# Performance work log

Hardware: AMD Instinct MI355X
Metric: run time of the kernel (lower is better)

Reference implementation:

```python
import jax, jax.numpy as jnp
from jax import lax
import numpy as np

DT_RANK = 2   # ceil(d_model=32 / 16)
D_STATE = 16

def conv3d(x, w, b=None):
    y = lax.conv_general_dilated(x, w, (1, 1, 1), 'SAME',
        dimension_numbers=('NCDHW', 'OIDHW', 'NCDHW'))
    if b is not None:
        y = y + b[None, :, None, None, None]
    return y

def instnorm(x, eps=1e-5):
    mu = x.mean((2, 3, 4), keepdims=True)
    var = x.var((2, 3, 4), keepdims=True)
    return (x - mu) / jnp.sqrt(var + eps)

def lrelu(x, a=0.1):
    return jnp.where(x >= 0, x, a * x)

def selective_scan(u, delta, A, Bm, Cm, D, z):
    # u, delta, z: (B,L,d); A: (d,n); Bm, Cm: (B,L,n); D: (d,)
    dA = jnp.exp(jnp.einsum('bld,dn->bldn', delta, A))
    dBu = jnp.einsum('bld,bln,bld->bldn', delta, Bm, u)
    def step(h, inp):
        dA_t, dBu_t, C_t = inp
        h = dA_t * h + dBu_t
        y = jnp.einsum('bdn,bn->bd', h, C_t)
        return h, y
    h0 = jnp.zeros(u.shape[:1] + A.shape, u.dtype)
    _, ys = lax.scan(step, h0, (dA.transpose(1, 0, 2, 3), dBu.transpose(1, 0, 2, 3), Cm.transpose(1, 0, 2)))
    y = ys.transpose(1, 0, 2) + u * D
    return y * jax.nn.silu(z)

def mamba_branch(xc, z, conv_w, conv_b, xproj_w, dtproj_w, dtproj_b, A_log, D):
    # xc: (B,d_in,L) pre-activation; z: (B,L,d_in)
    d = xc.shape[1]
    xp = jnp.pad(xc, ((0, 0), (0, 0), (conv_w.shape[-1] - 1, 0)))  # causal depthwise conv1d
    xp = lax.conv_general_dilated(xp, conv_w[:, None, :], (1,), 'VALID',
        dimension_numbers=('NCH', 'OIH', 'NCH'), feature_group_count=d)
    xt = jax.nn.silu(xp + conv_b[None, :, None]).transpose(0, 2, 1)  # (B,L,d)
    x_dbl = xt @ xproj_w.T
    dt = x_dbl[..., :DT_RANK]
    Bm = x_dbl[..., DT_RANK:DT_RANK + D_STATE]
    Cm = x_dbl[..., DT_RANK + D_STATE:]
    delta = jax.nn.softplus(dt @ dtproj_w.T + dtproj_b)
    A = -jnp.exp(A_log)
    return selective_scan(xt, delta, A, Bm, Cm, D, z)

def reference(x, ln_g, ln_b, in_proj_w, conv1d_w, conv1d_bias, x_proj_w, dt_proj_w, dt_proj_bias, A_log, D_f, conv1db_w, conv1db_bias, x_projb_w, dt_projb_w, dt_projb_bias, Ab_log, D_b, out_proj_w, cp1_w, cp1_b, elk1_w, elk1_b, elk2_w, elk2_b, elk3_w, elk3_b, elk4_w, elk4_b, elk5_w, elk5_b, cp2_w, cp2_b, atten_w, conv1_w, conv2_w, conv2_b):
    B, C = x.shape[:2]
    img = x.shape[2:]
    L = img[0] * img[1] * img[2]
    x_conv, x_m = jnp.split(x, 2, axis=1)
    # --- Mamba branch (bimamba v2) ---
    xm = x_m.reshape(B, C // 2, L).transpose(0, 2, 1)  # (B,L,d_model)
    mu = xm.mean(-1, keepdims=True)
    var = xm.var(-1, keepdims=True)
    xm = (xm - mu) / jnp.sqrt(var + 1e-5) * ln_g + ln_b
    xz = xm @ in_proj_w.T  # (B,L,2*d_in)
    d_in = xz.shape[-1] // 2
    xi = xz[..., :d_in].transpose(0, 2, 1)  # (B,d_in,L)
    z = xz[..., d_in:]                       # (B,L,d_in)
    y_f = mamba_branch(xi, z, conv1d_w, conv1d_bias, x_proj_w, dt_proj_w, dt_proj_bias, A_log, D_f)
    y_b = mamba_branch(xi[:, :, ::-1], z[:, ::-1], conv1db_w, conv1db_bias, x_projb_w, dt_projb_w, dt_projb_bias, Ab_log, D_b)
    y = (y_f + y_b[:, ::-1]) @ out_proj_w.T  # (B,L,d_model)
    x_mamba = y.transpose(0, 2, 1).reshape(B, C // 2, *img)
    # --- conv path (ConvInsBlock -> ELK -> IN/LReLU -> ConvInsBlock) ---
    h = lrelu(instnorm(conv3d(x_conv, cp1_w, cp1_b)))
    e = jnp.concatenate([conv3d(h, elk1_w, elk1_b), conv3d(h, elk2_w, elk2_b),
                         conv3d(h, elk3_w, elk3_b), conv3d(h, elk4_w, elk4_b)], axis=1)
    h = conv3d(e, elk5_w, elk5_b) + h
    h = lrelu(instnorm(h))
    h = lrelu(instnorm(conv3d(h, cp2_w, cp2_b)))
    # --- fusion with channel shuffle + double-sigmoid channel attention ---
    xcat = jnp.concatenate([h, x_mamba], axis=1)
    fused = xcat.reshape(B, 2, C // 2, *img).transpose(0, 2, 1, 3, 4, 5).reshape(B, C, *img)
    pooled = fused.mean((2, 3, 4), keepdims=True)
    attn = jax.nn.sigmoid(jax.nn.sigmoid(conv3d(pooled, atten_w)))  # sigmoid applied twice, as in source
    fused = conv3d(fused * attn, conv1_w)
    attn2 = jax.nn.sigmoid(conv3d(xcat, conv2_w, conv2_b))
    return fused * attn2

def setup_inputs():
    ks = iter(jax.random.split(jax.random.key(0), 64))
    def nrm(shape, s=0.05):
        return jax.random.normal(next(ks), shape, jnp.float32) * s
    dim, div, d_in = 64, 32, 64
    A_init = jnp.tile(jnp.log(jnp.arange(1, D_STATE + 1, dtype=jnp.float32))[None, :], (d_in, 1))
    inp = {
        'x': jax.random.normal(next(ks), (1, dim, 32, 32, 16), jnp.float32),
        'ln_g': jnp.ones((div,), jnp.float32),
        'ln_b': jnp.zeros((div,), jnp.float32),
        'in_proj_w': nrm((2 * d_in, div)),
        'conv1d_w': nrm((d_in, 4), 0.2),
        'conv1d_bias': nrm((d_in,), 0.1),
        'x_proj_w': nrm((DT_RANK + 2 * D_STATE, d_in)),
        'dt_proj_w': nrm((d_in, DT_RANK), 0.5),
        'dt_proj_bias': jax.random.uniform(next(ks), (d_in,), jnp.float32, -4.0, -2.0),
        'A_log': A_init,
        'D_f': jnp.ones((d_in,), jnp.float32),
        'conv1db_w': nrm((d_in, 4), 0.2),
        'conv1db_bias': nrm((d_in,), 0.1),
        'x_projb_w': nrm((DT_RANK + 2 * D_STATE, d_in)),
        'dt_projb_w': nrm((d_in, DT_RANK), 0.5),
        'dt_projb_bias': jax.random.uniform(next(ks), (d_in,), jnp.float32, -4.0, -2.0),
        'Ab_log': A_init,
        'D_b': jnp.ones((d_in,), jnp.float32),
        'out_proj_w': nrm((div, d_in)),
        'cp1_w': nrm((div, div, 1, 1, 1)),
        'cp1_b': nrm((div,)),
        'elk1_w': nrm((div // 2, div, 3, 3, 3)),
        'elk1_b': nrm((div // 2,)),
        'elk2_w': nrm((div // 2, div, 5, 1, 1)),
        'elk2_b': nrm((div // 2,)),
        'elk3_w': nrm((div // 2, div, 1, 5, 1)),
        'elk3_b': nrm((div // 2,)),
        'elk4_w': nrm((div // 2, div, 1, 1, 5)),
        'elk4_b': nrm((div // 2,)),
        'elk5_w': nrm((div, 2 * div, 1, 1, 1)),
        'elk5_b': nrm((div,)),
        'cp2_w': nrm((div, div, 1, 1, 1)),
        'cp2_b': nrm((div,)),
        'atten_w': nrm((dim, dim, 1, 1, 1)),
        'conv1_w': nrm((dim, dim, 1, 1, 1)),
        'conv2_w': nrm((1, dim, 1, 1, 1)),
        'conv2_b': nrm((1,)),
    }
    return inp
```

## Files before the change

### kernel.cpp

```cpp
#include <hip/hip_runtime.h>
#include <math.h>

constexpr int L  = 16384;
constexpr int LC = 64;
constexpr int NC = 256;

constexpr int PX = 20, PY = 36, PZ = 36;
constexpr int PSY = PX;
constexpr int PSZ = PY*PX;
constexpr int PCH = PZ*PSZ;

constexpr int TSX = 24;
constexpr int TSZ = 20*TSX;

__device__ __forceinline__ float sigm(float x){ return 1.0f/(1.0f+__expf(-x)); }
__device__ __forceinline__ float softplus_(float x){ return (x>20.0f)? x : log1pf(__expf(x)); }

__device__ __forceinline__ void block_accum2(float s, float s2, float* g0, float* g1){
    #pragma unroll
    for (int m=1;m<64;m<<=1){ s += __shfl_xor(s,m,64); s2 += __shfl_xor(s2,m,64); }
    __shared__ float red[16];
    int lane = threadIdx.x & 63, wid = threadIdx.x >> 6;
    if (lane==0){ red[wid]=s; red[8+wid]=s2; }
    __syncthreads();
    if (threadIdx.x==0){
        int nw = blockDim.x >> 6;
        float a=0.f,b=0.f;
        for (int i=0;i<nw;i++){ a+=red[i]; b+=red[8+i]; }
        atomicAdd(g0,a); atomicAdd(g1,b);
    }
}


__global__ __launch_bounds__(256,2)
void k_ln_proj(const float* __restrict__ x, const float* __restrict__ g,
               const float* __restrict__ b, const float* __restrict__ w,
               float* __restrict__ xi, float* __restrict__ z)
{
    __shared__ float xn[64][33];
    __shared__ float wt[32][36];
    int t  = threadIdx.x;
    int lq = t>>2, dc = t&3;
    int l  = blockIdx.x*64 + lq;
    int c0 = dc*8;
    int j0b = blockIdx.y*32;

    #pragma unroll
    for (int k=0;k<4;k++){
        int idx = t + k*256;
        int j = idx>>5, c = idx&31;
        wt[c][j] = w[(j0b+j)*32+c];
    }

    float xv[8]; float s=0.f, s2=0.f;
    #pragma unroll
    for (int cc=0;cc<8;cc++){
        float v = x[(32+c0+cc)*L + l];
        xv[cc]=v; s+=v; s2+=v*v;
    }
    #pragma unroll
    for (int m=1;m<4;m<<=1){ s += __shfl_xor(s,m,64); s2 += __shfl_xor(s2,m,64); }
    float mu  = s*(1.0f/32.0f);
    float var = s2*(1.0f/32.0f) - mu*mu;
    float inv = rsqrtf(var + 1e-5f);
    #pragma unroll
    for (int cc=0;cc<8;cc++)
        xn[lq][c0+cc] = (xv[cc]-mu)*inv*g[c0+cc] + b[c0+cc];
    __syncthreads();

    float acc[8];
    #pragma unroll
    for (int jj=0;jj<8;jj++) acc[jj]=0.f;
    #pragma unroll 4
    for (int c=0;c<32;c++){
        float uv = xn[lq][c];
        float4 w0 = *reinterpret_cast<const float4*>(&wt[c][dc*8]);
        float4 w1 = *reinterpret_cast<const float4*>(&wt[c][dc*8+4]);
        acc[0]+=w0.x*uv; acc[1]+=w0.y*uv; acc[2]+=w0.z*uv; acc[3]+=w0.w*uv;
        acc[4]+=w1.x*uv; acc[5]+=w1.y*uv; acc[6]+=w1.z*uv; acc[7]+=w1.w*uv;
    }
    int j0 = j0b + dc*8;
    if (j0 < 64){
        #pragma unroll
        for (int jj=0;jj<8;jj++) xi[(j0+jj)*L+l] = acc[jj];
    } else {
        #pragma unroll
        for (int q=0;q<2;q++)
            *reinterpret_cast<float4*>(z + l*64 + (j0-64) + q*4) =
                make_float4(acc[q*4], acc[q*4+1], acc[q*4+2], acc[q*4+3]);
    }
}

__global__ __launch_bounds__(256,2)
void k_conv_proj(const float* __restrict__ xi,
    const float* __restrict__ cwf, const float* __restrict__ cbf,
    const float* __restrict__ xwf, const float* __restrict__ dwf, const float* __restrict__ dbf,
    const float* __restrict__ cwb, const float* __restrict__ cbb,
    const float* __restrict__ xwb, const float* __restrict__ dwb, const float* __restrict__ dbb,
    float* __restrict__ uf, float* __restrict__ dlf, float* __restrict__ Bfp, float* __restrict__ Cfp,
    float* __restrict__ ub, float* __restrict__ dlb, float* __restrict__ Bbp, float* __restrict__ Cbp)
{
    __shared__ float uls[64][65];
    __shared__ float xwt[64][36];
    int t  = threadIdx.x;
    int lq = t>>2, dc = t&3;
    int l  = blockIdx.x*64 + lq;
    int d0 = dc*16;
    int gd = blockIdx.y;
    const float* cw = gd? cwb:cwf; const float* cb = gd? cbb:cbf;
    const float* xw = gd? xwb:xwf; const float* dw = gd? dwb:dwf; const float* db = gd? dbb:dbf;
    float* up = gd? ub:uf; float* dp = gd? dlb:dlf;
    float* Bp = gd? Bbp:Bfp; float* Cp = gd? Cbp:Cfp;

    #pragma unroll
    for (int k=0;k<9;k++){
        int idx = t + k*256;
        if (idx < 34*64){
            int r = idx>>6, c = idx&63;
            xwt[c][r] = xw[idx];
        }
    }

    float u16[16];
    #pragma unroll
    for (int dd=0; dd<16; dd++){
        int d = d0+dd;
        float s = cb[d];
        #pragma unroll
        for (int k=0;k<4;k++){
            int j = l-3+k;
            float v = 0.0f;
            if (j>=0) v = xi[d*L + (gd ? (L-1-j) : j)];
            s += cw[d*4+k]*v;
        }
        float u = s*sigm(s);
        u16[dd] = u;
        uls[lq][d] = u;
    }
    #pragma unroll
    for (int q=0;q<4;q++)
        *reinterpret_cast<float4*>(up + l*64 + d0 + q*4) =
            make_float4(u16[q*4], u16[q*4+1], u16[q*4+2], u16[q*4+3]);
    __syncthreads();

    float acc[8]; float t0=0.f, t1=0.f;
    #pragma unroll
    for (int jj=0;jj<8;jj++) acc[jj]=0.f;
    int rb = 2 + dc*8;
    #pragma unroll 4
    for (int c=0;c<64;c++){
        float uv = uls[lq][c];
        float2 d01 = *reinterpret_cast<const float2*>(&xwt[c][0]);
        t0 += d01.x*uv; t1 += d01.y*uv;
        float2 p0 = *reinterpret_cast<const float2*>(&xwt[c][rb]);
        float2 p1 = *reinterpret_cast<const float2*>(&xwt[c][rb+2]);
        float2 p2 = *reinterpret_cast<const float2*>(&xwt[c][rb+4]);
        float2 p3 = *reinterpret_cast<const float2*>(&xwt[c][rb+6]);
        acc[0]+=p0.x*uv; acc[1]+=p0.y*uv; acc[2]+=p1.x*uv; acc[3]+=p1.y*uv;
        acc[4]+=p2.x*uv; acc[5]+=p2.y*uv; acc[6]+=p3.x*uv; acc[7]+=p3.y*uv;
    }
    float* BC = (dc<2)? (Bp + l*16 + dc*8) : (Cp + l*16 + (dc-2)*8);
    *reinterpret_cast<float4*>(BC)   = make_float4(acc[0],acc[1],acc[2],acc[3]);
    *reinterpret_cast<float4*>(BC+4) = make_float4(acc[4],acc[5],acc[6],acc[7]);

    float dl16[16];
    #pragma unroll
    for (int dd=0; dd<16; dd++){
        int d = d0+dd;
        float tt = t0*dw[d*2] + t1*dw[d*2+1] + db[d];
        dl16[dd] = softplus_(tt);
    }
    #pragma unroll
    for (int q=0;q<4;q++)
        *reinterpret_cast<float4*>(dp + l*64 + d0 + q*4) =
            make_float4(dl16[q*4], dl16[q*4+1], dl16[q*4+2], dl16[q*4+3]);
}

__global__ void k_scan1(const float* __restrict__ dlf, const float* __restrict__ Bf, const float* __restrict__ ufp,
                        const float* __restrict__ dlb, const float* __restrict__ Bb, const float* __restrict__ ubp,
                        const float* __restrict__ Af, const float* __restrict__ Ab,
                        float* __restrict__ chA, float* __restrict__ chB)
{
    int tid = threadIdx.x;
    int c = blockIdx.x, gd = blockIdx.y;
    const float* dl = gd? dlb:dlf; const float* Bv = gd? Bb:Bf; const float* u = gd? ubp:ufp;
    float A = -__expf((gd? Ab:Af)[tid]);
    int d = tid>>4, n = tid&15;
    float h=0.f, p=1.f;
    int base = c*LC;
    #pragma unroll 4
    for (int i=0;i<LC;i++){
        int l = base+i;
        float dv = dl[l*64+d];
        float da = __expf(dv*A);
        float bu = dv * Bv[l*16+n] * u[l*64+d];
        h = da*h + bu;
        p *= da;
    }
    int o = (gd*NC + c)*1024 + tid;
    chA[o]=p; chB[o]=h;
}

__global__ void k_scan_agg(const float* __restrict__ chA, const float* __restrict__ chB,
                           float* __restrict__ hst)
{
    int tid = threadIdx.x; int gd = blockIdx.x;
    float h=0.f;
    #pragma unroll 8
    for (int c=0;c<NC;c++){
        int o = (gd*NC + c)*1024 + tid;
        hst[o]=h;
        h = chA[o]*h + chB[o];
    }
}

__global__ void k_scan2(const float* __restrict__ dlf, const float* __restrict__ Bf,
                        const float* __restrict__ Cf, const float* __restrict__ ufp,
                        const float* __restrict__ dlb, const float* __restrict__ Bb,
                        const float* __restrict__ Cb, const float* __restrict__ ubp,
                        const float* __restrict__ Af, const float* __restrict__ Ab,
                        const float* __restrict__ Dfp, const float* __restrict__ Dbp,
                        const float* __restrict__ hst,
                        float* __restrict__ yf, float* __restrict__ yb)
{
    int tid = threadIdx.x;
    int c = blockIdx.x, gd = blockIdx.y;
    const float* dl = gd? dlb:dlf; const float* Bv = gd? Bb:Bf;
    const float* Cv = gd? Cb:Cf;  const float* u  = gd? ubp:ufp;
    float A = -__expf((gd? Ab:Af)[tid]);
    int d = tid>>4, n = tid&15;
    float Dd = (gd? Dbp:Dfp)[d];
    float h = hst[(gd*NC + c)*1024 + tid];
    int base = c*LC;
    for (int i=0;i<LC;i++){
        int l = base+i;
        float dv = dl[l*64+d];
        float uu = u[l*64+d];
        float da = __expf(dv*A);
        h = da*h + dv * Bv[l*16+n] * uu;
        float t = h * Cv[l*16+n];
        t += __shfl_xor(t,1,16); t += __shfl_xor(t,2,16);
        t += __shfl_xor(t,4,16); t += __shfl_xor(t,8,16);
        if (n==0){
            float r = t + uu*Dd;
            if (gd) yb[(L-1-l)*64+d] = r;
            else    yf[l*64+d]       = r;
        }
    }
}

__global__ __launch_bounds__(256,2)
void k_combine(const float* __restrict__ yf, const float* __restrict__ yb,
               const float* __restrict__ z, const float* __restrict__ opw,
               float* __restrict__ xm)
{
    __shared__ float yls[64][65];
    __shared__ float ot[64][36];
    int t  = threadIdx.x;
    int lq = t>>2, dc = t&3;
    int l  = blockIdx.x*64 + lq;
    int d0 = dc*16;

    #pragma unroll
    for (int k=0;k<8;k++){
        int idx = t + k*256;
        int j = idx>>6, c = idx&63;
        ot[c][j] = opw[idx];
    }

    #pragma unroll
    for (int q=0;q<4;q++){
        float4 a = *reinterpret_cast<const float4*>(yf + l*64 + d0 + q*4);
        float4 bq= *reinterpret_cast<const float4*>(yb + l*64 + d0 + q*4);
        float4 zq= *reinterpret_cast<const float4*>(z  + l*64 + d0 + q*4);
        yls[lq][d0+q*4+0] = (a.x+bq.x)*(zq.x*sigm(zq.x));
        yls[lq][d0+q*4+1] = (a.y+bq.y)*(zq.y*sigm(zq.y));
        yls[lq][d0+q*4+2] = (a.z+bq.z)*(zq.z*sigm(zq.z));
        yls[lq][d0+q*4+3] = (a.w+bq.w)*(zq.w*sigm(zq.w));
    }
    __syncthreads();

    float acc[8];
    #pragma unroll
    for (int jj=0;jj<8;jj++) acc[jj]=0.f;
    #pragma unroll 4
    for (int c=0;c<64;c++){
        float uv = yls[lq][c];
        float4 w0 = *reinterpret_cast<const float4*>(&ot[c][dc*8]);
        float4 w1 = *reinterpret_cast<const float4*>(&ot[c][dc*8+4]);
        acc[0]+=w0.x*uv; acc[1]+=w0.y*uv; acc[2]+=w0.z*uv; acc[3]+=w0.w*uv;
        acc[4]+=w1.x*uv; acc[5]+=w1.y*uv; acc[6]+=w1.z*uv; acc[7]+=w1.w*uv;
    }
    #pragma unroll
    for (int jj=0;jj<8;jj++) xm[(dc*8+jj)*L+l] = acc[jj];
}


__global__ void k_conv1x1(const float* __restrict__ in, const float* __restrict__ w,
                          const float* __restrict__ b, float* __restrict__ out,
                          float* __restrict__ st)
{
    int oc = blockIdx.x; int l0 = blockIdx.y*(L/8);
    float s=0.f, s2=0.f;
    for (int l=l0+threadIdx.x; l<l0+L/8; l+=256){
        float acc = b[oc];
        #pragma unroll
        for (int ic=0;ic<32;ic++) acc += w[oc*32+ic]*in[ic*L+l];
        out[oc*L+l]=acc; s+=acc; s2+=acc*acc;
    }
    block_accum2(s,s2, st+oc, st+32+oc);
}

__global__ void k_norm(float* __restrict__ buf, const float* __restrict__ st)
{
    int oc = blockIdx.x; int l0 = blockIdx.y*(L/8);
    float mu  = st[oc]*(1.0f/(float)L);
    float var = st[32+oc]*(1.0f/(float)L) - mu*mu;
    float inv = rsqrtf(var + 1e-5f);
    for (int l=l0+threadIdx.x; l<l0+L/8; l+=256){
        float v = (buf[oc*L+l]-mu)*inv;
        buf[oc*L+l] = (v>=0.0f)? v : 0.1f*v;
    }
}

__global__ void k_norm_pad(float* __restrict__ buf, const float* __restrict__ st,
                           float* __restrict__ pad)
{
    int oc = blockIdx.x; int l0 = blockIdx.y*(L/8);
    float mu  = st[oc]*(1.0f/(float)L);
    float var = st[32+oc]*(1.0f/(float)L) - mu*mu;
    float inv = rsqrtf(var + 1e-5f);
    for (int l=l0+threadIdx.x; l<l0+L/8; l+=256){
        float v = (buf[oc*L+l]-mu)*inv;
        v = (v>=0.0f)? v : 0.1f*v;
        buf[oc*L+l] = v;
        int zx = l>>9, yy=(l>>4)&31, xx=l&15;
        pad[oc*PCH + (zx+2)*PSZ + (yy+2)*PSY + (xx+2)] = v;
    }
}

__global__ __launch_bounds__(256,2)
void k_elk(const float* __restrict__ hp,
           const float* __restrict__ w1, const float* __restrict__ b1,
           const float* __restrict__ w2, const float* __restrict__ b2,
           const float* __restrict__ w3, const float* __restrict__ b3,
           const float* __restrict__ w4, const float* __restrict__ b4,
           float* __restrict__ e)
{
    __shared__ float tile[2][5*TSZ];
    __shared__ float ws1[1728];
    __shared__ float ws2[320], ws3[320], ws4[320];
    int t  = threadIdx.x;
    int b  = blockIdx.x;
    int z0 = b>>1, yh = (b&1)*16;
    int ty = t>>4, tx = t&15;
    int l  = z0*512 + (yh+ty)*16 + tx;
    int oc0 = blockIdx.y*2;

    {
        const float* g1 = w1 + oc0*864;
        #pragma unroll
        for (int k=0;k<7;k++){ int idx=t+k*256; if (idx<1728) ws1[idx]=g1[idx]; }
        const float* g2 = w2 + oc0*160;
        const float* g3 = w3 + oc0*160;
        const float* g4 = w4 + oc0*160;
        #pragma unroll
        for (int k=0;k<2;k++){
            int idx=t+k*256;
            if (idx<320){ ws2[idx]=g2[idx]; ws3[idx]=g3[idx]; ws4[idx]=g4[idx]; }
        }
    }

    const float* src0 = hp + z0*PSZ + yh*PSY;
    int co = 2*TSZ + (ty+2)*TSX + (tx+2);

    float a1[2],a2[2],a3[2],a4[2];
    #pragma unroll
    for (int o=0;o<2;o++){ a1[o]=b1[oc0+o]; a2[o]=b2[oc0+o]; a3[o]=b3[oc0+o]; a4[o]=b4[oc0+o]; }

    #pragma unroll
    for (int k=0;k<8;k++){
        int idx = t + k*256;
        if (idx < 2000){
            int zz = idx/400, rem = idx - zz*400;
            int yy = rem/20,  xx  = rem - yy*20;
            tile[0][zz*TSZ + yy*TSX + xx] = src0[zz*PSZ + rem];
        }
    }
    __syncthreads();

    for (int ic=0; ic<32; ic++){
        int cur = ic&1;
        float r[8];
        if (ic<31){
            const float* srcn = src0 + (ic+1)*PCH;
            #pragma unroll
            for (int k=0;k<8;k++){
                int idx = t + k*256;
                int zz = idx/400;
                r[k] = (idx<2000) ? srcn[zz*PSZ + (idx - zz*400)] : 0.0f;
            }
        }
        const float* tl = tile[cur];
        float v[27];
        #pragma unroll
        for (int dz=0;dz<3;dz++)
        #pragma unroll
        for (int dy=0;dy<3;dy++)
        #pragma unroll
        for (int dx=0;dx<3;dx++)
            v[(dz*3+dy)*3+dx] = tl[co + (dz-1)*TSZ + (dy-1)*TSX + (dx-1)];
        float z5[5], y5[5], x5[5];
        #pragma unroll
        for (int q=0;q<5;q++){
            z5[q] = tl[co + (q-2)*TSZ];
            y5[q] = tl[co + (q-2)*TSX];
            x5[q] = tl[co + (q-2)];
        }
        #pragma unroll
        for (int o=0;o<2;o++){
            const float* wp1 = ws1 + (o*32+ic)*27;
            float a = a1[o];
            #pragma unroll
            for (int q=0;q<27;q++) a += wp1[q]*v[q];
            a1[o]=a;
            const float* wp2 = ws2 + (o*32+ic)*5;
            const float* wp3 = ws3 + (o*32+ic)*5;
            const float* wp4 = ws4 + (o*32+ic)*5;
            float s2a=a2[o], s3a=a3[o], s4a=a4[o];
            #pragma unroll
            for (int q=0;q<5;q++){
                s2a += wp2[q]*z5[q];
                s3a += wp3[q]*y5[q];
                s4a += wp4[q]*x5[q];
            }
            a2[o]=s2a; a3[o]=s3a; a4[o]=s4a;
        }
        if (ic<31){
            #pragma unroll
            for (int k=0;k<8;k++){
                int idx = t + k*256;
                if (idx < 2000){
                    int zz = idx/400, rem = idx - zz*400;
                    int yy = rem/20,  xx  = rem - yy*20;
                    tile[cur^1][zz*TSZ + yy*TSX + xx] = r[k];
                }
            }
            __syncthreads();
        }
    }
    #pragma unroll
    for (int o=0;o<2;o++){
        e[(oc0+o)*L+l]      = a1[o];
        e[(16+oc0+o)*L+l]   = a2[o];
        e[(32+oc0+o)*L+l]   = a3[o];
        e[(48+oc0+o)*L+l]   = a4[o];
    }
}

__global__ void k_elk5(const float* __restrict__ e, const float* __restrict__ hres,
                       const float* __restrict__ w, const float* __restrict__ b,
                       float* __restrict__ h2, float* __restrict__ st)
{
    int oc = blockIdx.x; int l0 = blockIdx.y*(L/8);
    float s=0.f, s2=0.f;
    for (int l=l0+threadIdx.x; l<l0+L/8; l+=256){
        float acc = b[oc];
        #pragma unroll
        for (int m=0;m<64;m++) acc += w[oc*64+m]*e[m*L+l];
        acc += hres[oc*L+l];
        h2[oc*L+l]=acc; s+=acc; s2+=acc*acc;
    }
    block_accum2(s,s2, st+oc, st+32+oc);
}


__global__ void k_pool(const float* __restrict__ h3, const float* __restrict__ xm,
                       float* __restrict__ pooled)
{
    int fc = blockIdx.x; int l0 = blockIdx.y*(L/8);
    const float* src = (fc&1) ? xm + (fc>>1)*L : h3 + (fc>>1)*L;
    float s=0.f;
    for (int l=l0+threadIdx.x; l<l0+L/8; l+=256) s += src[l];
    #pragma unroll
    for (int m=1;m<64;m<<=1) s += __shfl_xor(s,m,64);
    __shared__ float red[4];
    int lane = threadIdx.x&63, wid = threadIdx.x>>6;
    if (lane==0) red[wid]=s;
    __syncthreads();
    if (threadIdx.x==0) atomicAdd(pooled+fc, red[0]+red[1]+red[2]+red[3]);
}

__global__ void k_attn(const float* __restrict__ pooled, const float* __restrict__ aw,
                       float* __restrict__ attn)
{
    __shared__ float pl[64];
    int t = threadIdx.x;
    pl[t] = pooled[t]*(1.0f/(float)L);
    __syncthreads();
    float acc=0.f;
    #pragma unroll
    for (int c=0;c<64;c++) acc += aw[t*64+c]*pl[c];
    attn[t] = sigm(sigm(acc));
}

__global__ __launch_bounds__(256,2)
void k_final(const float* __restrict__ h3, const float* __restrict__ xm,
             const float* __restrict__ attn, const float* __restrict__ w1,
             const float* __restrict__ c2w, const float* __restrict__ c2b,
             float* __restrict__ out)
{
    __shared__ float w1s[64][20];
    __shared__ float sA[64], sG[64];
    int t = threadIdx.x;
    int o0 = blockIdx.y*16;

    #pragma unroll
    for (int k=0;k<4;k++){
        int idx = t + k*256;
        int o = idx>>6, c = idx&63;
        w1s[c][o] = w1[(o0+o)*64 + c];
    }
    if (t < 64){ sA[t] = attn[t]; sG[t] = c2w[t]; }
    __syncthreads();

    int l = blockIdx.x*blockDim.x + t;
    float acc[16];
    #pragma unroll
    for (int o=0;o<16;o++) acc[o]=0.f;
    float a2 = c2b[0];
    #pragma unroll 4
    for (int i=0;i<32;i++){
        float hv = h3[i*L+l];
        float xv = xm[i*L+l];
        a2 += sG[i]*hv + sG[32+i]*xv;
        float fh = hv*sA[2*i];
        float fx = xv*sA[2*i+1];
        float4 p0 = *reinterpret_cast<const float4*>(&w1s[2*i][0]);
        float4 p1 = *reinterpret_cast<const float4*>(&w1s[2*i][4]);
        float4 p2 = *reinterpret_cast<const float4*>(&w1s[2*i][8]);
        float4 p3 = *reinterpret_cast<const float4*>(&w1s[2*i][12]);
        float4 q0 = *reinterpret_cast<const float4*>(&w1s[2*i+1][0]);
        float4 q1 = *reinterpret_cast<const float4*>(&w1s[2*i+1][4]);
        float4 q2 = *reinterpret_cast<const float4*>(&w1s[2*i+1][8]);
        float4 q3 = *reinterpret_cast<const float4*>(&w1s[2*i+1][12]);
        acc[0] += p0.x*fh + q0.x*fx;  acc[1] += p0.y*fh + q0.y*fx;
        acc[2] += p0.z*fh + q0.z*fx;  acc[3] += p0.w*fh + q0.w*fx;
        acc[4] += p1.x*fh + q1.x*fx;  acc[5] += p1.y*fh + q1.y*fx;
        acc[6] += p1.z*fh + q1.z*fx;  acc[7] += p1.w*fh + q1.w*fx;
        acc[8] += p2.x*fh + q2.x*fx;  acc[9] += p2.y*fh + q2.y*fx;
        acc[10]+= p2.z*fh + q2.z*fx;  acc[11]+= p2.w*fh + q2.w*fx;
        acc[12]+= p3.x*fh + q3.x*fx;  acc[13]+= p3.y*fh + q3.y*fx;
        acc[14]+= p3.z*fh + q3.z*fx;  acc[15]+= p3.w*fh + q3.w*fx;
    }
    float at2 = sigm(a2);
    #pragma unroll
    for (int o=0;o<16;o++) out[(o0+o)*L+l] = acc[o]*at2;
}


extern "C" void kernel_launch(void* const* d_in, const int* in_sizes, int n_in,
                              void* d_out, int out_size, void* d_ws, size_t ws_size,
                              hipStream_t stream)
{
    const float* x         = (const float*)d_in[0];
    const float* ln_g      = (const float*)d_in[1];
    const float* ln_b      = (const float*)d_in[2];
    const float* in_proj_w = (const float*)d_in[3];
    const float* conv1d_w  = (const float*)d_in[4];
    const float* conv1d_b  = (const float*)d_in[5];
    const float* x_proj_w  = (const float*)d_in[6];
    const float* dt_proj_w = (const float*)d_in[7];
    const float* dt_proj_b = (const float*)d_in[8];
    const float* A_log     = (const float*)d_in[9];
    const float* D_f       = (const float*)d_in[10];
    const float* conv1db_w = (const float*)d_in[11];
    const float* conv1db_b = (const float*)d_in[12];
    const float* x_projb_w = (const float*)d_in[13];
    const float* dt_projb_w= (const float*)d_in[14];
    const float* dt_projb_b= (const float*)d_in[15];
    const float* Ab_log    = (const float*)d_in[16];
    const float* D_b       = (const float*)d_in[17];
    const float* out_proj_w= (const float*)d_in[18];
    const float* cp1_w     = (const float*)d_in[19];
    const float* cp1_b     = (const float*)d_in[20];
    const float* elk1_w    = (const float*)d_in[21];
    const float* elk1_b    = (const float*)d_in[22];
    const float* elk2_w    = (const float*)d_in[23];
    const float* elk2_b    = (const float*)d_in[24];
    const float* elk3_w    = (const float*)d_in[25];
    const float* elk3_b    = (const float*)d_in[26];
    const float* elk4_w    = (const float*)d_in[27];
    const float* elk4_b    = (const float*)d_in[28];
    const float* elk5_w    = (const float*)d_in[29];
    const float* elk5_b    = (const float*)d_in[30];
    const float* cp2_w     = (const float*)d_in[31];
    const float* cp2_b     = (const float*)d_in[32];
    const float* atten_w   = (const float*)d_in[33];
    const float* conv1_w   = (const float*)d_in[34];
    const float* conv2_w   = (const float*)d_in[35];
    const float* conv2_b   = (const float*)d_in[36];

    float* ws = (float*)d_ws;
    float* XI  = ws + 0;
    float* Z   = ws + 1048576;
    float* UF  = ws + 2097152;
    float* UB  = ws + 3145728;
    float* DLF = ws + 4194304;
    float* DLB = ws + 5242880;
    float* BF  = ws + 6291456;
    float* CF  = ws + 6553600;
    float* BB  = ws + 6815744;
    float* CB  = ws + 7077888;
    float* CHA = ws + 7340032;
    float* CHB = ws + 7864320;
    float* HST = ws + 8388608;
    float* YF  = ws + 8912896;
    float* YB  = ws + 9961472;
    float* XM  = ws + 11010048;
    float* H1  = ws + 11534336;
    float* E4  = ws + 12058624;
    float* H2  = ws + 13107200;
    float* H3  = ws + 13631488;
    float* ST  = ws + 14155776;
    float* H1P = XI;

    hipMemsetAsync(ST, 0, 256*sizeof(float), stream);

    k_ln_proj<<<dim3(L/64,4), 256, 0, stream>>>(x, ln_g, ln_b, in_proj_w, XI, Z);
    k_conv_proj<<<dim3(L/64,2), 256, 0, stream>>>(XI,
        conv1d_w, conv1d_b, x_proj_w, dt_proj_w, dt_proj_b,
        conv1db_w, conv1db_b, x_projb_w, dt_projb_w, dt_projb_b,
        UF, DLF, BF, CF, UB, DLB, BB, CB);
    k_scan1<<<dim3(NC,2), 1024, 0, stream>>>(DLF, BF, UF, DLB, BB, UB, A_log, Ab_log, CHA, CHB);
    k_scan_agg<<<2, 1024, 0, stream>>>(CHA, CHB, HST);
    k_scan2<<<dim3(NC,2), 1024, 0, stream>>>(DLF, BF, CF, UF, DLB, BB, CB, UB,
                                             A_log, Ab_log, D_f, D_b, HST, YF, YB);
    k_combine<<<dim3(L/64), 256, 0, stream>>>(YF, YB, Z, out_proj_w, XM);

    k_conv1x1<<<dim3(32,8), 256, 0, stream>>>(x, cp1_w, cp1_b, H1, ST);
    hipMemsetAsync(H1P, 0, 32*PCH*sizeof(float), stream);
    k_norm_pad<<<dim3(32,8), 256, 0, stream>>>(H1, ST, H1P);
    k_elk<<<dim3(L/256,8), 256, 0, stream>>>(H1P, elk1_w, elk1_b, elk2_w, elk2_b,
                                             elk3_w, elk3_b, elk4_w, elk4_b, E4);
    k_elk5<<<dim3(32,8), 256, 0, stream>>>(E4, H1, elk5_w, elk5_b, H2, ST+64);
    k_norm<<<dim3(32,8), 256, 0, stream>>>(H2, ST+64);
    k_conv1x1<<<dim3(32,8), 256, 0, stream>>>(H2, cp2_w, cp2_b, H3, ST+128);
    k_norm<<<dim3(32,8), 256, 0, stream>>>(H3, ST+128);

    k_pool<<<dim3(64,8), 256, 0, stream>>>(H3, XM, ST+192);
    k_attn<<<1, 64, 0, stream>>>(ST+192, atten_w, ST+256);
    k_final<<<dim3(L/256,4), 256, 0, stream>>>(H3, XM, ST+256, conv1_w, conv2_w, conv2_b,
                                               (float*)d_out);
}
```

Measured before the change: 382.1 us.

## Split ELK conv input channels across two blocks and sum partials in elk5

Splits the 32 input channels of the ELK multi-branch convolution over a new grid z dimension of two halves. Each half writes partial sums to a separate buffer (reusing the YB workspace), and k_elk5 adds the two partials before the 1x1 projection. Weights are now read straight from global memory instead of being staged in shared memory. The tile load is simplified to a linear, padded index, and launch bounds rise to four blocks per SM. The aim is more blocks and more occupancy for the conv stage, at the cost of an extra partial-sum buffer that elk5 must read.

```diff
diff --git a/kernel.cpp b/kernel.cpp
--- a/kernel.cpp
+++ b/kernel.cpp
@@ -12,6 +12,7 @@
 
 constexpr int TSX = 24;
 constexpr int TSZ = 20*TSX;
+constexpr int TILE_N = 5*TSZ;
 
 __device__ __forceinline__ float sigm(float x){ return 1.0f/(1.0f+__expf(-x)); }
 __device__ __forceinline__ float softplus_(float x){ return (x>20.0f)? x : log1pf(__expf(x)); }
@@ -339,66 +340,61 @@
     }
 }
 
-__global__ __launch_bounds__(256,2)
+__global__ __launch_bounds__(256,4)
 void k_elk(const float* __restrict__ hp,
            const float* __restrict__ w1, const float* __restrict__ b1,
            const float* __restrict__ w2, const float* __restrict__ b2,
            const float* __restrict__ w3, const float* __restrict__ b3,
            const float* __restrict__ w4, const float* __restrict__ b4,
-           float* __restrict__ e)
-{
-    __shared__ float tile[2][5*TSZ];
-    __shared__ float ws1[1728];
-    __shared__ float ws2[320], ws3[320], ws4[320];
+           float* __restrict__ e, float* __restrict__ eb)
+{
+    __shared__ float tile[2][TILE_N];
     int t  = threadIdx.x;
     int b  = blockIdx.x;
     int z0 = b>>1, yh = (b&1)*16;
     int ty = t>>4, tx = t&15;
     int l  = z0*512 + (yh+ty)*16 + tx;
     int oc0 = blockIdx.y*2;
-
-    {
-        const float* g1 = w1 + oc0*864;
-        #pragma unroll
-        for (int k=0;k<7;k++){ int idx=t+k*256; if (idx<1728) ws1[idx]=g1[idx]; }
-        const float* g2 = w2 + oc0*160;
-        const float* g3 = w3 + oc0*160;
-        const float* g4 = w4 + oc0*160;
-        #pragma unroll
-        for (int k=0;k<2;k++){
-            int idx=t+k*256;
-            if (idx<320){ ws2[idx]=g2[idx]; ws3[idx]=g3[idx]; ws4[idx]=g4[idx]; }
-        }
-    }
-
-    const float* src0 = hp + z0*PSZ + yh*PSY;
+    int ich = blockIdx.z;
+    const float* src0 = hp + ich*16*PCH + z0*PSZ + yh*PSY;
     int co = 2*TSZ + (ty+2)*TSX + (tx+2);
 
     float a1[2],a2[2],a3[2],a4[2];
     #pragma unroll
-    for (int o=0;o<2;o++){ a1[o]=b1[oc0+o]; a2[o]=b2[oc0+o]; a3[o]=b3[oc0+o]; a4[o]=b4[oc0+o]; }
-
-    #pragma unroll
-    for (int k=0;k<8;k++){
+    for (int o=0;o<2;o++){
+        a1[o] = ich? 0.f : b1[oc0+o];
+        a2[o] = ich? 0.f : b2[oc0+o];
+        a3[o] = ich? 0.f : b3[oc0+o];
+        a4[o] = ich? 0.f : b4[oc0+o];
+    }
+
+    #pragma unroll
+    for (int k=0;k<10;k++){
         int idx = t + k*256;
-        if (idx < 2000){
-            int zz = idx/400, rem = idx - zz*400;
-            int yy = rem/20,  xx  = rem - yy*20;
-            tile[0][zz*TSZ + yy*TSX + xx] = src0[zz*PSZ + rem];
-        }
-    }
-    __syncthreads();
-
-    for (int ic=0; ic<32; ic++){
-        int cur = ic&1;
-        float r[8];
-        if (ic<31){
-            const float* srcn = src0 + (ic+1)*PCH;
+        if (idx < TILE_N){
+            int zz = idx/TSZ, rem = idx - zz*TSZ;
+            int yy = rem/TSX, xx = rem - yy*TSX;
+            tile[0][idx] = (xx<20) ? src0[zz*PSZ + yy*PSY + xx] : 0.0f;
+        }
+    }
+    __syncthreads();
+
+    for (int ic16=0; ic16<16; ic16++){
+        int ic = ich*16 + ic16;
+        int cur = ic16&1;
+        float r[10];
+        if (ic16<15){
+            const float* srcn = src0 + (ic16+1)*PCH;
             #pragma unroll
-            for (int k=0;k<8;k++){
+            for (int k=0;k<10;k++){
                 int idx = t + k*256;
-                int zz = idx/400;
-                r[k] = (idx<2000) ? srcn[zz*PSZ + (idx - zz*400)] : 0.0f;
+                float v = 0.0f;
+                if (idx < TILE_N){
+                    int zz = idx/TSZ, rem = idx - zz*TSZ;
+                    int yy = rem/TSX, xx = rem - yy*TSX;
+                    if (xx<20) v = srcn[zz*PSZ + yy*PSY + xx];
+                }
+                r[k] = v;
             }
         }
         const float* tl = tile[cur];
@@ -419,14 +415,14 @@
         }
         #pragma unroll
         for (int o=0;o<2;o++){
-            const float* wp1 = ws1 + (o*32+ic)*27;
+            const float* wp1 = w1 + ((oc0+o)*32+ic)*27;
             float a = a1[o];
             #pragma unroll
             for (int q=0;q<27;q++) a += wp1[q]*v[q];
             a1[o]=a;
-            const float* wp2 = ws2 + (o*32+ic)*5;
-            const float* wp3 = ws3 + (o*32+ic)*5;
-            const float* wp4 = ws4 + (o*32+ic)*5;
+            const float* wp2 = w2 + ((oc0+o)*32+ic)*5;
+            const float* wp3 = w3 + ((oc0+o)*32+ic)*5;
+            const float* wp4 = w4 + ((oc0+o)*32+ic)*5;
             float s2a=a2[o], s3a=a3[o], s4a=a4[o];
             #pragma unroll
             for (int q=0;q<5;q++){
@@ -436,29 +432,27 @@
             }
             a2[o]=s2a; a3[o]=s3a; a4[o]=s4a;
         }
-        if (ic<31){
+        if (ic16<15){
             #pragma unroll
-            for (int k=0;k<8;k++){
+            for (int k=0;k<10;k++){
                 int idx = t + k*256;
-                if (idx < 2000){
-                    int zz = idx/400, rem = idx - zz*400;
-                    int yy = rem/20,  xx  = rem - yy*20;
-                    tile[cur^1][zz*TSZ + yy*TSX + xx] = r[k];
-                }
+                if (idx < TILE_N) tile[cur^1][idx] = r[k];
             }
             __syncthreads();
         }
     }
+    float* eo = ich ? eb : e;
     #pragma unroll
     for (int o=0;o<2;o++){
-        e[(oc0+o)*L+l]      = a1[o];
-        e[(16+oc0+o)*L+l]   = a2[o];
-        e[(32+oc0+o)*L+l]   = a3[o];
-        e[(48+oc0+o)*L+l]   = a4[o];
-    }
-}
-
-__global__ void k_elk5(const float* __restrict__ e, const float* __restrict__ hres,
+        eo[(oc0+o)*L+l]      = a1[o];
+        eo[(16+oc0+o)*L+l]   = a2[o];
+        eo[(32+oc0+o)*L+l]   = a3[o];
+        eo[(48+oc0+o)*L+l]   = a4[o];
+    }
+}
+
+__global__ void k_elk5(const float* __restrict__ e, const float* __restrict__ ebp,
+                       const float* __restrict__ hres,
                        const float* __restrict__ w, const float* __restrict__ b,
                        float* __restrict__ h2, float* __restrict__ st)
 {
@@ -467,7 +461,7 @@
     for (int l=l0+threadIdx.x; l<l0+L/8; l+=256){
         float acc = b[oc];
         #pragma unroll
-        for (int m=0;m<64;m++) acc += w[oc*64+m]*e[m*L+l];
+        for (int m=0;m<64;m++) acc += w[oc*64+m]*(e[m*L+l]+ebp[m*L+l]);
         acc += hres[oc*L+l];
         h2[oc*L+l]=acc; s+=acc; s2+=acc*acc;
     }
@@ -624,6 +618,7 @@
     float* H3  = ws + 13631488;
     float* ST  = ws + 14155776;
     float* H1P = XI;
+    float* E4B = YB;
 
     hipMemsetAsync(ST, 0, 256*sizeof(float), stream);
 
@@ -641,9 +636,9 @@
     k_conv1x1<<<dim3(32,8), 256, 0, stream>>>(x, cp1_w, cp1_b, H1, ST);
     hipMemsetAsync(H1P, 0, 32*PCH*sizeof(float), stream);
     k_norm_pad<<<dim3(32,8), 256, 0, stream>>>(H1, ST, H1P);
-    k_elk<<<dim3(L/256,8), 256, 0, stream>>>(H1P, elk1_w, elk1_b, elk2_w, elk2_b,
-                                             elk3_w, elk3_b, elk4_w, elk4_b, E4);
-    k_elk5<<<dim3(32,8), 256, 0, stream>>>(E4, H1, elk5_w, elk5_b, H2, ST+64);
+    k_elk<<<dim3(L/256,8,2), 256, 0, stream>>>(H1P, elk1_w, elk1_b, elk2_w, elk2_b,
+                                               elk3_w, elk3_b, elk4_w, elk4_b, E4, E4B);
+    k_elk5<<<dim3(32,8), 256, 0, stream>>>(E4, E4B, H1, elk5_w, elk5_b, H2, ST+64);
     k_norm<<<dim3(32,8), 256, 0, stream>>>(H2, ST+64);
     k_conv1x1<<<dim3(32,8), 256, 0, stream>>>(H2, cp2_w, cp2_b, H3, ST+128);
     k_norm<<<dim3(32,8), 256, 0, stream>>>(H3, ST+128);
```

After: 479.1 us. +25.4%, slower.
